# Kernel optimization log

Hardware: AMD Instinct MI355X
Metric: run time of the kernel (lower is better)

The kernel has to match this reference:

```python
import jax, jax.numpy as jnp
import numpy as np
import math

B = 2; T = 512; ND = 256; NDAYS = 24; STRIDE = 4; KLEN = 14
DM = ND * KLEN          # 3584, d_model after unfolding
NLAYERS = 2; DSTATE = 16; DCONV = 4; EXPAND = 2
DI = EXPAND * DM        # 7168 d_inner
DTR = math.ceil(DM / 16)  # 224 dt_rank
NCLS = 41
LOUT = (T - KLEN) // STRIDE + 1  # 125


def setup_inputs():
    key = jax.random.key(0)
    ks = jax.random.split(key, 12)
    f32 = jnp.float32
    neuralInput = jax.random.normal(ks[0], (B, T, ND), f32)
    dayIdx = jax.random.randint(ks[1], (B,), 0, NDAYS)
    # day-specific linear init: identity weight, zero bias (as in BaseDecoder)
    day_w = jnp.tile(jnp.eye(ND, dtype=f32)[None], (NDAYS, 1, 1))
    day_b = jnp.zeros((NDAYS, 1, ND), f32)
    norm_w = jnp.ones((NLAYERS, DM), f32)
    norm_b = jnp.zeros((NLAYERS, DM), f32)
    in_proj_w = 0.02 * jax.random.normal(ks[2], (NLAYERS, 2 * DI, DM), f32)
    conv_w = 0.2 * jax.random.normal(ks[3], (NLAYERS, DI, DCONV), f32)  # depthwise
    conv_b = jnp.zeros((NLAYERS, DI), f32)
    x_proj_w = 0.02 * jax.random.normal(ks[4], (NLAYERS, DTR + 2 * DSTATE, DI), f32)
    s = DTR ** -0.5
    dt_proj_w = jax.random.uniform(ks[5], (NLAYERS, DI, DTR), f32, -s, s)
    # dt bias init: inverse-softplus of dt ~ LogUniform[1e-3, 1e-1]
    dt = jnp.exp(jax.random.uniform(ks[6], (NLAYERS, DI), f32) * (math.log(0.1) - math.log(0.001)) + math.log(0.001))
    dt = jnp.clip(dt, 1e-4, None)
    dt_proj_b = dt + jnp.log(-jnp.expm1(-dt))
    A_log = jnp.broadcast_to(jnp.log(jnp.arange(1, DSTATE + 1, dtype=f32)), (NLAYERS, DI, DSTATE)).copy()
    D_param = jnp.ones((NLAYERS, DI), f32)
    out_proj_w = 0.02 * jax.random.normal(ks[7], (NLAYERS, DM, DI), f32)
    normf_w = jnp.ones((DM,), f32)
    normf_b = jnp.zeros((DM,), f32)
    fc_w = 0.02 * jax.random.normal(ks[8], (NCLS, DM), f32)
    fc_b = jnp.zeros((NCLS,), f32)
    return dict(neuralInput=neuralInput, day_w=day_w, day_b=day_b, norm_w=norm_w, norm_b=norm_b,
                in_proj_w=in_proj_w, conv_w=conv_w, conv_b=conv_b, x_proj_w=x_proj_w,
                dt_proj_w=dt_proj_w, dt_proj_b=dt_proj_b, A_log=A_log, D_param=D_param,
                out_proj_w=out_proj_w, normf_w=normf_w, normf_b=normf_b, fc_w=fc_w, fc_b=fc_b,
                dayIdx=dayIdx)


def _layernorm(x, w, b):
    mu = x.mean(-1, keepdims=True)
    v = jnp.var(x, -1, keepdims=True)
    return (x - mu) * jax.lax.rsqrt(v + 1e-5) * w + b


def _mamba(h, ipw, cw, cb, xpw, dtw, dtb, Alog, Dp, opw):
    # h: (B, L, DM) -> (B, L, DM); unidirectional Mamba, use_fast_path=False math
    Bb, L, _ = h.shape
    xz = h @ ipw.T                              # (B, L, 2*DI)
    x, z = xz[..., :DI], xz[..., DI:]
    # depthwise causal conv1d, kernel DCONV, left pad DCONV-1, truncated to L
    xp = jnp.pad(x, ((0, 0), (DCONV - 1, 0), (0, 0)))
    xc = cb + sum(xp[:, j:j + L, :] * cw[:, j] for j in range(DCONV))
    x = jax.nn.silu(xc)
    x_dbl = x @ xpw.T                           # (B, L, DTR + 2*N)
    dt = x_dbl[..., :DTR]
    Bc = x_dbl[..., DTR:DTR + DSTATE]
    Cc = x_dbl[..., DTR + DSTATE:]
    delta = jax.nn.softplus(dt @ dtw.T + dtb)   # (B, L, DI), delta_softplus=True
    A = -jnp.exp(Alog)                          # (DI, N)
    dA = jnp.exp(delta[..., None] * A)          # (B, L, DI, N)
    dBu = (delta * x)[..., None] * Bc[:, :, None, :]  # (B, L, DI, N)

    def step(hst, inp):
        a, bu, c = inp
        hst = a * hst + bu                      # (B, DI, N)
        return hst, jnp.einsum('bdn,bn->bd', hst, c)

    h0 = jnp.zeros((Bb, DI, DSTATE), h.dtype)
    _, ys = jax.lax.scan(step, h0, (dA.transpose(1, 0, 2, 3), dBu.transpose(1, 0, 2, 3), Cc.transpose(1, 0, 2)))
    y = ys.transpose(1, 0, 2) + x * Dp          # skip term D*u
    y = y * jax.nn.silu(z)                      # gated output
    return y @ opw.T


def reference(neuralInput, day_w, day_b, norm_w, norm_b, in_proj_w, conv_w, conv_b, x_proj_w,
              dt_proj_w, dt_proj_b, A_log, D_param, out_proj_w, normf_w, normf_b, fc_w, fc_b, dayIdx):
    # --- BaseDecoder.forward_preprocessing (gaussianSmoothWidth = 0) ---
    t = jnp.einsum('btd,bdk->btk', neuralInput, day_w[dayIdx]) + day_b[dayIdx]
    t = t / (1.0 + jnp.abs(t))                  # Softsign
    idx = jnp.arange(LOUT)[:, None] * STRIDE + jnp.arange(KLEN)[None, :]
    win = t[:, idx, :]                          # (B, LOUT, KLEN, ND)
    # torch Unfold feature ordering: channel-major then kernel position -> d*KLEN + j
    h = win.transpose(0, 1, 3, 2).reshape(t.shape[0], LOUT, DM)
    # --- stacked Mamba blocks (pre-norm residual) ---
    residual = None
    for i in range(NLAYERS):
        residual = h if residual is None else h + residual
        hn = _layernorm(residual, norm_w[i], norm_b[i])
        h = _mamba(hn, in_proj_w[i], conv_w[i], conv_b[i], x_proj_w[i], dt_proj_w[i],
                   dt_proj_b[i], A_log[i], D_param[i], out_proj_w[i])
    residual = h + residual
    hn = _layernorm(residual, normf_w, normf_b)
    return hn @ fc_w.T + fc_b                   # (B, LOUT, NCLS)
```

## Files before the change

### kernel.cpp

```cpp
#include <hip/hip_runtime.h>
#include <hip/hip_bf16.h>
#include <math.h>

#define BATCH   2
#define TSEQ    512
#define NDIM    256
#define STRIDE_ 4
#define KLEN    14
#define DM      3584
#define DI      7168
#define DTR     224
#define DSTATE  16
#define NCLS    41
#define LOUT    125
#define LPAD    128
#define MROWS   256

typedef __attribute__((ext_vector_type(8))) short bf8_t;
typedef __attribute__((ext_vector_type(4))) float f4_t;

__device__ inline unsigned bfpair(float a, float b) {
    unsigned ua = __builtin_bit_cast(unsigned, a);
    unsigned ub = __builtin_bit_cast(unsigned, b);
    ua = (ua + 0x7fffu + ((ua >> 16) & 1u)) >> 16;
    ub = (ub + 0x7fffu + ((ub >> 16) & 1u)) >> 16;
    return ua | (ub << 16);
}
__device__ inline uint4 pack8(float4 a, float4 b) {
    return make_uint4(bfpair(a.x, a.y), bfpair(a.z, a.w),
                      bfpair(b.x, b.y), bfpair(b.z, b.w));
}

__global__ void day_proj(const float* __restrict__ nI, const float* __restrict__ dw,
                         const float* __restrict__ db, const int* __restrict__ dayIdx,
                         float* __restrict__ t_full) {
    int bi = blockIdx.x;
    int b = bi >> 9;
    int di = dayIdx[b];
    int tid = threadIdx.x;
    __shared__ float a_sh[256];
    a_sh[tid] = nI[(size_t)bi * 256 + tid];
    __syncthreads();
    const float* w = dw + (size_t)di * 65536;
    float acc = db[(size_t)di * 256 + tid];
    #pragma unroll 8
    for (int d = 0; d < 256; ++d) acc = fmaf(a_sh[d], w[d * 256 + tid], acc);
    t_full[(size_t)bi * 256 + tid] = acc / (1.f + fabsf(acc));
}

__global__ void window_k(const float* __restrict__ t_full, float* __restrict__ res) {
    int bl = blockIdx.x;
    int b = bl >> 7, l = bl & 127;
    size_t m = (size_t)b * LPAD + l;
    if (l >= LOUT) {
        for (int c = threadIdx.x; c < DM; c += 256) res[m * DM + c] = 0.f;
        return;
    }
    for (int c = threadIdx.x; c < DM; c += 256) {
        int d = c / KLEN, j = c - d * KLEN;
        res[m * DM + c] = t_full[((size_t)b * TSEQ + l * STRIDE_ + j) * 256 + d];
    }
}

__global__ void ln_pack(const float* __restrict__ res, const float* __restrict__ w,
                        const float* __restrict__ b, short* __restrict__ hnp) {
    int m = blockIdx.x, tid = threadIdx.x;
    const float* row = res + (size_t)m * DM;
    float s = 0.f, ss = 0.f;
    for (int c = tid; c < DM; c += 256) { float v = row[c]; s += v; ss += v * v; }
    #pragma unroll
    for (int o = 32; o; o >>= 1) { s += __shfl_xor(s, o); ss += __shfl_xor(ss, o); }
    __shared__ float sm[8];
    int wid = tid >> 6;
    if ((tid & 63) == 0) { sm[wid] = s; sm[4 + wid] = ss; }
    __syncthreads();
    s = sm[0] + sm[1] + sm[2] + sm[3];
    ss = sm[4] + sm[5] + sm[6] + sm[7];
    float mu = s * (1.f / DM);
    float var = ss * (1.f / DM) - mu * mu;
    float rs = rsqrtf(var + 1e-5f);
    for (int G = tid; G < DM / 8; G += 256) {
        float4 f0 = *(const float4*)(row + G * 8);
        float4 f1 = *(const float4*)(row + G * 8 + 4);
        float4 w0 = *(const float4*)(w + G * 8);
        float4 w1 = *(const float4*)(w + G * 8 + 4);
        float4 b0 = *(const float4*)(b + G * 8);
        float4 b1 = *(const float4*)(b + G * 8 + 4);
        f0.x = (f0.x - mu) * rs * w0.x + b0.x; f0.y = (f0.y - mu) * rs * w0.y + b0.y;
        f0.z = (f0.z - mu) * rs * w0.z + b0.z; f0.w = (f0.w - mu) * rs * w0.w + b0.w;
        f1.x = (f1.x - mu) * rs * w1.x + b1.x; f1.y = (f1.y - mu) * rs * w1.y + b1.y;
        f1.z = (f1.z - mu) * rs * w1.z + b1.z; f1.w = (f1.w - mu) * rs * w1.w + b1.w;
        *(uint4*)&hnp[((size_t)G * 256 + m) * 8] = pack8(f0, f1);
    }
}

__global__ void pack_rows(const float* __restrict__ src, int lda, int nG,
                          short* __restrict__ dst) {
    int m = blockIdx.x;
    const float* row = src + (size_t)m * lda;
    for (int G = threadIdx.x; G < nG; G += 256) {
        float4 f0 = *(const float4*)(row + G * 8);
        float4 f1 = *(const float4*)(row + G * 8 + 4);
        *(uint4*)&dst[((size_t)G * 256 + m) * 8] = pack8(f0, f1);
    }
}

__global__ void zero_k(float* __restrict__ p) {
    size_t i = (size_t)(blockIdx.x * 256 + threadIdx.x) * 4;
    *(float4*)(p + i) = make_float4(0.f, 0.f, 0.f, 0.f);
}

template <int EPI>
__global__ __launch_bounds__(256)
void gemm_mfma(const short* __restrict__ Ap, const float* __restrict__ W, int ldw,
               float* __restrict__ C, int ldc, int kSteps,
               const float* __restrict__ bias) {
    __shared__ __align__(16) short a_sh[2][4][2056];
    __shared__ __align__(16) short w_sh[2][4][520];
    const int tid = threadIdx.x;
    const int wz = tid >> 6, lane = tid & 63;
    const int g = lane >> 4, i16 = lane & 15;
    const int n0 = blockIdx.x * 64;
    const int sBeg = blockIdx.z * kSteps, sEnd = sBeg + kSteps;
    const int wr = tid >> 3;
    const int wq = tid & 7;

    f4_t acc[4][4];
    #pragma unroll
    for (int r = 0; r < 4; ++r)
        #pragma unroll
        for (int c = 0; c < 4; ++c) acc[r][c] = (f4_t){0.f, 0.f, 0.f, 0.f};

    const short* arow = Ap + (size_t)tid * 8;
    const float* wbase  = W + (size_t)(n0 + wr) * ldw + wq * 4;
    const float* wbase2 = wbase + (size_t)32 * ldw;

    float4 wv0 = *(const float4*)(wbase  + (size_t)sBeg * 32);
    float4 wv1 = *(const float4*)(wbase2 + (size_t)sBeg * 32);
    #pragma unroll
    for (int it = 0; it < 4; ++it)
        __builtin_amdgcn_global_load_lds(
            (const __attribute__((address_space(1))) unsigned int*)(arow + (size_t)(sBeg * 4 + it) * 2048),
            (__attribute__((address_space(3))) unsigned int*)&a_sh[0][it][tid * 8], 16, 0, 0);
    {
        uint2 p0 = {bfpair(wv0.x, wv0.y), bfpair(wv0.z, wv0.w)};
        *(uint2*)&w_sh[0][wq >> 1][wr * 8 + (wq & 1) * 4] = p0;
        uint2 p1 = {bfpair(wv1.x, wv1.y), bfpair(wv1.z, wv1.w)};
        *(uint2*)&w_sh[0][wq >> 1][(wr + 32) * 8 + (wq & 1) * 4] = p1;
    }
    int s1 = (sBeg + 1 < sEnd) ? sBeg + 1 : sEnd - 1;
    wv0 = *(const float4*)(wbase  + (size_t)s1 * 32);
    wv1 = *(const float4*)(wbase2 + (size_t)s1 * 32);

    for (int s = sBeg; s < sEnd; ++s) {
        const int cur = (s - sBeg) & 1, nxt = cur ^ 1;
        __syncthreads();
        if (s + 1 < sEnd) {
            #pragma unroll
            for (int it = 0; it < 4; ++it)
                __builtin_amdgcn_global_load_lds(
                    (const __attribute__((address_space(1))) unsigned int*)(arow + (size_t)((s + 1) * 4 + it) * 2048),
                    (__attribute__((address_space(3))) unsigned int*)&a_sh[nxt][it][tid * 8], 16, 0, 0);
            uint2 p0 = {bfpair(wv0.x, wv0.y), bfpair(wv0.z, wv0.w)};
            *(uint2*)&w_sh[nxt][wq >> 1][wr * 8 + (wq & 1) * 4] = p0;
            uint2 p1 = {bfpair(wv1.x, wv1.y), bfpair(wv1.z, wv1.w)};
            *(uint2*)&w_sh[nxt][wq >> 1][(wr + 32) * 8 + (wq & 1) * 4] = p1;
            int s2 = (s + 2 < sEnd) ? s + 2 : sEnd - 1;
            wv0 = *(const float4*)(wbase  + (size_t)s2 * 32);
            wv1 = *(const float4*)(wbase2 + (size_t)s2 * 32);
        }
        bf8_t af[4], wf[4];
        #pragma unroll
        for (int r = 0; r < 4; ++r)
            af[r] = *(const bf8_t*)&a_sh[cur][g][(wz * 64 + r * 16 + i16) * 8];
        #pragma unroll
        for (int c = 0; c < 4; ++c)
            wf[c] = *(const bf8_t*)&w_sh[cur][g][(c * 16 + i16) * 8];
        #pragma unroll
        for (int r = 0; r < 4; ++r)
            #pragma unroll
            for (int c = 0; c < 4; ++c)
                acc[r][c] = __builtin_amdgcn_mfma_f32_16x16x32_bf16(af[r], wf[c], acc[r][c], 0, 0, 0);
    }

    float bv[4];
    if (EPI == 1) {
        #pragma unroll
        for (int c = 0; c < 4; ++c) bv[c] = bias[n0 + c * 16 + i16];
    }
    #pragma unroll
    for (int r = 0; r < 4; ++r) {
        #pragma unroll
        for (int c = 0; c < 4; ++c) {
            int n = n0 + c * 16 + i16;
            #pragma unroll
            for (int v = 0; v < 4; ++v) {
                int m = wz * 64 + r * 16 + g * 4 + v;
                float val = acc[r][c][v];
                if (EPI == 0) {
                    C[(size_t)m * ldc + n] = val;
                } else if (EPI == 1) {
                    val += bv[c];
                    C[(size_t)m * ldc + n] = (val > 20.f) ? val : log1pf(expf(val));
                } else {
                    atomicAdd(&C[(size_t)m * ldc + n], val);
                }
            }
        }
    }
}

__global__ void conv_silu_pack(const float* __restrict__ xz, const float* __restrict__ cw,
                               const float* __restrict__ cb, float* __restrict__ xq,
                               short* __restrict__ xqp) {
    int bl = blockIdx.x;
    int b = bl / 125, l = bl % 125;
    size_t m = (size_t)b * LPAD + l;
    for (int c0 = threadIdx.x * 8; c0 < DI; c0 += 2048) {
        float v[8];
        float4 cb0 = *(const float4*)(cb + c0);
        float4 cb1 = *(const float4*)(cb + c0 + 4);
        v[0] = cb0.x; v[1] = cb0.y; v[2] = cb0.z; v[3] = cb0.w;
        v[4] = cb1.x; v[5] = cb1.y; v[6] = cb1.z; v[7] = cb1.w;
        #pragma unroll
        for (int j = 0; j < 4; ++j) {
            int lj = l - 3 + j;
            if (lj < 0) continue;
            const float* xr = xz + ((size_t)b * LPAD + lj) * (2 * DI) + c0;
            float4 x0 = *(const float4*)xr;
            float4 x1 = *(const float4*)(xr + 4);
            float xa[8] = {x0.x, x0.y, x0.z, x0.w, x1.x, x1.y, x1.z, x1.w};
            #pragma unroll
            for (int k = 0; k < 8; ++k)
                v[k] = fmaf(xa[k], cw[(c0 + k) * 4 + j], v[k]);
        }
        float4 o0, o1;
        #pragma unroll
        for (int k = 0; k < 8; ++k) {
            float sv = v[k] / (1.f + expf(-v[k]));
            if (k < 4) (&o0.x)[k] = sv; else (&o1.x)[k - 4] = sv;
        }
        *(float4*)(xq + m * DI + c0) = o0;
        *(float4*)(xq + m * DI + c0 + 4) = o1;
        *(uint4*)&xqp[(((size_t)c0 / 8) * 256 + m) * 8] = pack8(o0, o1);
    }
}

union F16u { float4 v4[4]; float f[16]; };

__global__ void scan_kernel(const float* __restrict__ delta, const float* __restrict__ xq,
                            const float* __restrict__ xdbl, const float* __restrict__ xz,
                            const float* __restrict__ Alog, const float* __restrict__ Dp,
                            float* __restrict__ y) {
    int c = blockIdx.x * 256 + threadIdx.x;
    int b = blockIdx.y;
    float As[DSTATE], st[DSTATE];
    #pragma unroll
    for (int s = 0; s < DSTATE; ++s) {
        As[s] = -expf(Alog[(size_t)c * DSTATE + s]);
        st[s] = 0.f;
    }
    float dp = Dp[c];
    size_t mb = (size_t)b * LPAD;
    float d_c = delta[mb * DI + c];
    float x_c = xq[mb * DI + c];
    float z_c = xz[mb * (2 * DI) + DI + c];
    F16u B_c, C_c;
    {
        const float4* p = (const float4*)(xdbl + mb * 256 + DTR);
        B_c.v4[0] = p[0]; B_c.v4[1] = p[1]; B_c.v4[2] = p[2]; B_c.v4[3] = p[3];
        C_c.v4[0] = p[4]; C_c.v4[1] = p[5]; C_c.v4[2] = p[6]; C_c.v4[3] = p[7];
    }
    for (int l = 0; l < LOUT; ++l) {
        float d_n = d_c, x_n = x_c, z_n = z_c;
        F16u B_n = B_c, C_n = C_c;
        if (l + 1 < LOUT) {
            size_t m = mb + l + 1;
            d_n = delta[m * DI + c];
            x_n = xq[m * DI + c];
            z_n = xz[m * (2 * DI) + DI + c];
            const float4* p = (const float4*)(xdbl + m * 256 + DTR);
            B_n.v4[0] = p[0]; B_n.v4[1] = p[1]; B_n.v4[2] = p[2]; B_n.v4[3] = p[3];
            C_n.v4[0] = p[4]; C_n.v4[1] = p[5]; C_n.v4[2] = p[6]; C_n.v4[3] = p[7];
        }
        float du = d_c * x_c;
        float yv = 0.f;
        #pragma unroll
        for (int s = 0; s < DSTATE; ++s) {
            st[s] = fmaf(expf(d_c * As[s]), st[s], du * B_c.f[s]);
            yv = fmaf(st[s], C_c.f[s], yv);
        }
        y[(mb + l) * DI + c] = (yv + x_c * dp) * (z_c / (1.f + expf(-z_c)));
        d_c = d_n; x_c = x_n; z_c = z_n; B_c = B_n; C_c = C_n;
    }
}

__global__ void ln_fc(const float* __restrict__ res, const float* __restrict__ wf,
                      const float* __restrict__ bf, const float* __restrict__ fcw,
                      const float* __restrict__ fcb, float* __restrict__ out) {
    __shared__ __align__(16) float hs[DM];
    __shared__ float sm[8];
    int bl = blockIdx.x;
    int b = bl / 125, l = bl % 125;
    size_t m = (size_t)b * LPAD + l;
    int tid = threadIdx.x;
    const float* row = res + m * DM;
    float s = 0.f, ss = 0.f;
    for (int c = tid; c < DM; c += 256) { float v = row[c]; s += v; ss += v * v; }
    #pragma unroll
    for (int o = 32; o; o >>= 1) { s += __shfl_xor(s, o); ss += __shfl_xor(ss, o); }
    int wid = tid >> 6;
    if ((tid & 63) == 0) { sm[wid] = s; sm[4 + wid] = ss; }
    __syncthreads();
    s = sm[0] + sm[1] + sm[2] + sm[3];
    ss = sm[4] + sm[5] + sm[6] + sm[7];
    float mu = s * (1.f / DM);
    float var = ss * (1.f / DM) - mu * mu;
    float rs = rsqrtf(var + 1e-5f);
    for (int c = tid; c < DM; c += 256) hs[c] = (row[c] - mu) * rs * wf[c] + bf[c];
    __syncthreads();
    int lane = tid & 63;
    for (int n = wid; n < NCLS; n += 4) {
        const float* wrow = fcw + (size_t)n * DM;
        float a0 = 0.f, a1 = 0.f, a2 = 0.f, a3 = 0.f;
        for (int k = lane; k < DM; k += 256) {
            a0 = fmaf(hs[k],       wrow[k],       a0);
            a1 = fmaf(hs[k + 64],  wrow[k + 64],  a1);
            a2 = fmaf(hs[k + 128], wrow[k + 128], a2);
            a3 = fmaf(hs[k + 192], wrow[k + 192], a3);
        }
        float acc = (a0 + a1) + (a2 + a3);
        #pragma unroll
        for (int o = 32; o; o >>= 1) acc += __shfl_xor(acc, o);
        if (lane == 0) out[((size_t)b * LOUT + l) * NCLS + n] = acc + fcb[n];
    }
}

extern "C" void kernel_launch(void* const* d_in, const int* in_sizes, int n_in,
                              void* d_out, int out_size, void* d_ws, size_t ws_size,
                              hipStream_t stream) {
    (void)in_sizes; (void)n_in; (void)out_size; (void)ws_size;
    const float* nI   = (const float*)d_in[0];
    const float* dw   = (const float*)d_in[1];
    const float* db   = (const float*)d_in[2];
    const float* nw   = (const float*)d_in[3];
    const float* nb   = (const float*)d_in[4];
    const float* ipw  = (const float*)d_in[5];
    const float* cw   = (const float*)d_in[6];
    const float* cb   = (const float*)d_in[7];
    const float* xpw  = (const float*)d_in[8];
    const float* dtw  = (const float*)d_in[9];
    const float* dtb  = (const float*)d_in[10];
    const float* Alog = (const float*)d_in[11];
    const float* Dp   = (const float*)d_in[12];
    const float* opw  = (const float*)d_in[13];
    const float* nfw  = (const float*)d_in[14];
    const float* nfb  = (const float*)d_in[15];
    const float* fcw  = (const float*)d_in[16];
    const float* fcb  = (const float*)d_in[17];
    const int*   dayI = (const int*)d_in[18];
    float* out = (float*)d_out;

    float* wsf = (float*)d_ws;
    float* t_full = wsf; wsf += 262144;
    float* res    = wsf; wsf += (size_t)MROWS * DM;
    float* xz     = wsf; wsf += (size_t)MROWS * 2 * DI;
    float* xq     = wsf; wsf += (size_t)MROWS * DI;
    float* xdbl   = wsf; wsf += (size_t)MROWS * 256;
    float* delta  = wsf; wsf += (size_t)MROWS * DI;
    float* yb     = wsf; wsf += (size_t)MROWS * DI;
    short* wss = (short*)wsf;
    short* hnp   = wss; wss += (size_t)MROWS * DM;
    short* xqp   = wss; wss += (size_t)MROWS * DI;
    short* xdblp = wss; wss += (size_t)MROWS * DTR;
    short* ybp   = wss; wss += (size_t)MROWS * DI;

    day_proj<<<dim3(BATCH * TSEQ), 256, 0, stream>>>(nI, dw, db, dayI, t_full);
    window_k<<<dim3(MROWS), 256, 0, stream>>>(t_full, res);

    for (int i = 0; i < 2; ++i) {
        ln_pack<<<dim3(MROWS), 256, 0, stream>>>(res, nw + (size_t)i * DM, nb + (size_t)i * DM, hnp);
        gemm_mfma<0><<<dim3(224, 1, 1), 256, 0, stream>>>(
            hnp, ipw + (size_t)i * 2 * DI * DM, DM, xz, 2 * DI, 112, nullptr);
        conv_silu_pack<<<dim3(BATCH * LOUT), 256, 0, stream>>>(
            xz, cw + (size_t)i * DI * 4, cb + (size_t)i * DI, xq, xqp);
        zero_k<<<dim3(64), 256, 0, stream>>>(xdbl);
        gemm_mfma<2><<<dim3(4, 1, 28), 256, 0, stream>>>(
            xqp, xpw + (size_t)i * 256 * DI, DI, xdbl, 256, 8, nullptr);
        pack_rows<<<dim3(MROWS), 256, 0, stream>>>(xdbl, 256, DTR / 8, xdblp);
        gemm_mfma<1><<<dim3(112, 1, 1), 256, 0, stream>>>(
            xdblp, dtw + (size_t)i * DI * DTR, DTR, delta, DI, 7, dtb + (size_t)i * DI);
        scan_kernel<<<dim3(DI / 256, BATCH), 256, 0, stream>>>(
            delta, xq, xdbl, xz, Alog + (size_t)i * DI * DSTATE, Dp + (size_t)i * DI, yb);
        pack_rows<<<dim3(MROWS), 256, 0, stream>>>(yb, DI, DI / 8, ybp);
        gemm_mfma<2><<<dim3(56, 1, 8), 256, 0, stream>>>(
            ybp, opw + (size_t)i * DM * DI, DI, res, DM, 28, nullptr);
    }

    ln_fc<<<dim3(BATCH * LOUT), 256, 0, stream>>>(res, nfw, nfb, fcw, fcb, out);
}
```

Before: 1.353 ms.

## Halve GEMM N-tile to 32 and split scan states across four threads

The MFMA GEMM gets an N-tile template parameter. All GEMMs now use 32-column tiles with twice as many blocks, and the out_proj split-K is reduced from 8 to 4. The selective scan now gives each channel's 16 states to 4 threads, which combine their partial outputs with shuffles, so it launches four times as many threads. Both changes aim to fill the GPU's compute units better on these small-M problems, at the cost of more weight-tile redundancy, lower MFMA work per block, and extra shuffle and load overhead in the scan.

```diff
diff --git a/kernel.cpp b/kernel.cpp
--- a/kernel.cpp
+++ b/kernel.cpp
@@ -110,33 +110,35 @@
     *(float4*)(p + i) = make_float4(0.f, 0.f, 0.f, 0.f);
 }
 
-template <int EPI>
+template <int EPI, int NT>
 __global__ __launch_bounds__(256)
 void gemm_mfma(const short* __restrict__ Ap, const float* __restrict__ W, int ldw,
                float* __restrict__ C, int ldc, int kSteps,
                const float* __restrict__ bias) {
+    constexpr int NC = NT / 16;
     __shared__ __align__(16) short a_sh[2][4][2056];
-    __shared__ __align__(16) short w_sh[2][4][520];
+    __shared__ __align__(16) short w_sh[2][4][NT * 8 + 8];
     const int tid = threadIdx.x;
     const int wz = tid >> 6, lane = tid & 63;
     const int g = lane >> 4, i16 = lane & 15;
-    const int n0 = blockIdx.x * 64;
+    const int n0 = blockIdx.x * NT;
     const int sBeg = blockIdx.z * kSteps, sEnd = sBeg + kSteps;
     const int wr = tid >> 3;
     const int wq = tid & 7;
 
-    f4_t acc[4][4];
+    f4_t acc[4][NC];
     #pragma unroll
     for (int r = 0; r < 4; ++r)
         #pragma unroll
-        for (int c = 0; c < 4; ++c) acc[r][c] = (f4_t){0.f, 0.f, 0.f, 0.f};
+        for (int c = 0; c < NC; ++c) acc[r][c] = (f4_t){0.f, 0.f, 0.f, 0.f};
 
     const short* arow = Ap + (size_t)tid * 8;
     const float* wbase  = W + (size_t)(n0 + wr) * ldw + wq * 4;
     const float* wbase2 = wbase + (size_t)32 * ldw;
 
-    float4 wv0 = *(const float4*)(wbase  + (size_t)sBeg * 32);
-    float4 wv1 = *(const float4*)(wbase2 + (size_t)sBeg * 32);
+    float4 wv0 = *(const float4*)(wbase + (size_t)sBeg * 32);
+    float4 wv1;
+    if constexpr (NT == 64) wv1 = *(const float4*)(wbase2 + (size_t)sBeg * 32);
     #pragma unroll
     for (int it = 0; it < 4; ++it)
         __builtin_amdgcn_global_load_lds(
@@ -145,12 +147,14 @@
     {
         uint2 p0 = {bfpair(wv0.x, wv0.y), bfpair(wv0.z, wv0.w)};
         *(uint2*)&w_sh[0][wq >> 1][wr * 8 + (wq & 1) * 4] = p0;
-        uint2 p1 = {bfpair(wv1.x, wv1.y), bfpair(wv1.z, wv1.w)};
-        *(uint2*)&w_sh[0][wq >> 1][(wr + 32) * 8 + (wq & 1) * 4] = p1;
+        if constexpr (NT == 64) {
+            uint2 p1 = {bfpair(wv1.x, wv1.y), bfpair(wv1.z, wv1.w)};
+            *(uint2*)&w_sh[0][wq >> 1][(wr + 32) * 8 + (wq & 1) * 4] = p1;
+        }
     }
     int s1 = (sBeg + 1 < sEnd) ? sBeg + 1 : sEnd - 1;
-    wv0 = *(const float4*)(wbase  + (size_t)s1 * 32);
-    wv1 = *(const float4*)(wbase2 + (size_t)s1 * 32);
+    wv0 = *(const float4*)(wbase + (size_t)s1 * 32);
+    if constexpr (NT == 64) wv1 = *(const float4*)(wbase2 + (size_t)s1 * 32);
 
     for (int s = sBeg; s < sEnd; ++s) {
         const int cur = (s - sBeg) & 1, nxt = cur ^ 1;
@@ -163,35 +167,37 @@
                     (__attribute__((address_space(3))) unsigned int*)&a_sh[nxt][it][tid * 8], 16, 0, 0);
             uint2 p0 = {bfpair(wv0.x, wv0.y), bfpair(wv0.z, wv0.w)};
             *(uint2*)&w_sh[nxt][wq >> 1][wr * 8 + (wq & 1) * 4] = p0;
-            uint2 p1 = {bfpair(wv1.x, wv1.y), bfpair(wv1.z, wv1.w)};
-            *(uint2*)&w_sh[nxt][wq >> 1][(wr + 32) * 8 + (wq & 1) * 4] = p1;
+            if constexpr (NT == 64) {
+                uint2 p1 = {bfpair(wv1.x, wv1.y), bfpair(wv1.z, wv1.w)};
+                *(uint2*)&w_sh[nxt][wq >> 1][(wr + 32) * 8 + (wq & 1) * 4] = p1;
+            }
             int s2 = (s + 2 < sEnd) ? s + 2 : sEnd - 1;
-            wv0 = *(const float4*)(wbase  + (size_t)s2 * 32);
-            wv1 = *(const float4*)(wbase2 + (size_t)s2 * 32);
-        }
-        bf8_t af[4], wf[4];
+            wv0 = *(const float4*)(wbase + (size_t)s2 * 32);
+            if constexpr (NT == 64) wv1 = *(const float4*)(wbase2 + (size_t)s2 * 32);
+        }
+        bf8_t af[4], wf[NC];
         #pragma unroll
         for (int r = 0; r < 4; ++r)
             af[r] = *(const bf8_t*)&a_sh[cur][g][(wz * 64 + r * 16 + i16) * 8];
         #pragma unroll
-        for (int c = 0; c < 4; ++c)
+        for (int c = 0; c < NC; ++c)
             wf[c] = *(const bf8_t*)&w_sh[cur][g][(c * 16 + i16) * 8];
         #pragma unroll
         for (int r = 0; r < 4; ++r)
             #pragma unroll
-            for (int c = 0; c < 4; ++c)
+            for (int c = 0; c < NC; ++c)
                 acc[r][c] = __builtin_amdgcn_mfma_f32_16x16x32_bf16(af[r], wf[c], acc[r][c], 0, 0, 0);
     }
 
-    float bv[4];
+    float bv[NC];
     if (EPI == 1) {
         #pragma unroll
-        for (int c = 0; c < 4; ++c) bv[c] = bias[n0 + c * 16 + i16];
+        for (int c = 0; c < NC; ++c) bv[c] = bias[n0 + c * 16 + i16];
     }
     #pragma unroll
     for (int r = 0; r < 4; ++r) {
         #pragma unroll
-        for (int c = 0; c < 4; ++c) {
+        for (int c = 0; c < NC; ++c) {
             int n = n0 + c * 16 + i16;
             #pragma unroll
             for (int v = 0; v < 4; ++v) {
@@ -246,51 +252,49 @@
     }
 }
 
-union F16u { float4 v4[4]; float f[16]; };
-
 __global__ void scan_kernel(const float* __restrict__ delta, const float* __restrict__ xq,
                             const float* __restrict__ xdbl, const float* __restrict__ xz,
                             const float* __restrict__ Alog, const float* __restrict__ Dp,
                             float* __restrict__ y) {
-    int c = blockIdx.x * 256 + threadIdx.x;
+    int tid = threadIdx.x;
+    int sg = tid & 3;
+    int c = blockIdx.x * 64 + (tid >> 2);
     int b = blockIdx.y;
-    float As[DSTATE], st[DSTATE];
-    #pragma unroll
-    for (int s = 0; s < DSTATE; ++s) {
-        As[s] = -expf(Alog[(size_t)c * DSTATE + s]);
-        st[s] = 0.f;
+    float As[4], st[4];
+    #pragma unroll
+    for (int k = 0; k < 4; ++k) {
+        As[k] = -expf(Alog[(size_t)c * DSTATE + sg * 4 + k]);
+        st[k] = 0.f;
     }
     float dp = Dp[c];
     size_t mb = (size_t)b * LPAD;
     float d_c = delta[mb * DI + c];
     float x_c = xq[mb * DI + c];
     float z_c = xz[mb * (2 * DI) + DI + c];
-    F16u B_c, C_c;
-    {
-        const float4* p = (const float4*)(xdbl + mb * 256 + DTR);
-        B_c.v4[0] = p[0]; B_c.v4[1] = p[1]; B_c.v4[2] = p[2]; B_c.v4[3] = p[3];
-        C_c.v4[0] = p[4]; C_c.v4[1] = p[5]; C_c.v4[2] = p[6]; C_c.v4[3] = p[7];
-    }
+    float4 B_c = *(const float4*)(xdbl + mb * 256 + DTR + sg * 4);
+    float4 C_c = *(const float4*)(xdbl + mb * 256 + DTR + DSTATE + sg * 4);
     for (int l = 0; l < LOUT; ++l) {
         float d_n = d_c, x_n = x_c, z_n = z_c;
-        F16u B_n = B_c, C_n = C_c;
+        float4 B_n = B_c, C_n = C_c;
         if (l + 1 < LOUT) {
             size_t m = mb + l + 1;
             d_n = delta[m * DI + c];
             x_n = xq[m * DI + c];
             z_n = xz[m * (2 * DI) + DI + c];
-            const float4* p = (const float4*)(xdbl + m * 256 + DTR);
-            B_n.v4[0] = p[0]; B_n.v4[1] = p[1]; B_n.v4[2] = p[2]; B_n.v4[3] = p[3];
-            C_n.v4[0] = p[4]; C_n.v4[1] = p[5]; C_n.v4[2] = p[6]; C_n.v4[3] = p[7];
+            B_n = *(const float4*)(xdbl + m * 256 + DTR + sg * 4);
+            C_n = *(const float4*)(xdbl + m * 256 + DTR + DSTATE + sg * 4);
         }
         float du = d_c * x_c;
         float yv = 0.f;
         #pragma unroll
-        for (int s = 0; s < DSTATE; ++s) {
-            st[s] = fmaf(expf(d_c * As[s]), st[s], du * B_c.f[s]);
-            yv = fmaf(st[s], C_c.f[s], yv);
-        }
-        y[(mb + l) * DI + c] = (yv + x_c * dp) * (z_c / (1.f + expf(-z_c)));
+        for (int k = 0; k < 4; ++k) {
+            st[k] = fmaf(expf(d_c * As[k]), st[k], du * (&B_c.x)[k]);
+            yv = fmaf(st[k], (&C_c.x)[k], yv);
+        }
+        yv += __shfl_xor(yv, 1);
+        yv += __shfl_xor(yv, 2);
+        if (sg == 0)
+            y[(mb + l) * DI + c] = (yv + x_c * dp) * (z_c / (1.f + expf(-z_c)));
         d_c = d_n; x_c = x_n; z_c = z_n; B_c = B_n; C_c = C_n;
     }
 }
@@ -380,21 +384,21 @@
 
     for (int i = 0; i < 2; ++i) {
         ln_pack<<<dim3(MROWS), 256, 0, stream>>>(res, nw + (size_t)i * DM, nb + (size_t)i * DM, hnp);
-        gemm_mfma<0><<<dim3(224, 1, 1), 256, 0, stream>>>(
+        gemm_mfma<0, 32><<<dim3(448, 1, 1), 256, 0, stream>>>(
             hnp, ipw + (size_t)i * 2 * DI * DM, DM, xz, 2 * DI, 112, nullptr);
         conv_silu_pack<<<dim3(BATCH * LOUT), 256, 0, stream>>>(
             xz, cw + (size_t)i * DI * 4, cb + (size_t)i * DI, xq, xqp);
         zero_k<<<dim3(64), 256, 0, stream>>>(xdbl);
-        gemm_mfma<2><<<dim3(4, 1, 28), 256, 0, stream>>>(
+        gemm_mfma<2, 32><<<dim3(8, 1, 28), 256, 0, stream>>>(
             xqp, xpw + (size_t)i * 256 * DI, DI, xdbl, 256, 8, nullptr);
         pack_rows<<<dim3(MROWS), 256, 0, stream>>>(xdbl, 256, DTR / 8, xdblp);
-        gemm_mfma<1><<<dim3(112, 1, 1), 256, 0, stream>>>(
+        gemm_mfma<1, 32><<<dim3(224, 1, 1), 256, 0, stream>>>(
             xdblp, dtw + (size_t)i * DI * DTR, DTR, delta, DI, 7, dtb + (size_t)i * DI);
-        scan_kernel<<<dim3(DI / 256, BATCH), 256, 0, stream>>>(
+        scan_kernel<<<dim3(DI / 64, BATCH), 256, 0, stream>>>(
             delta, xq, xdbl, xz, Alog + (size_t)i * DI * DSTATE, Dp + (size_t)i * DI, yb);
         pack_rows<<<dim3(MROWS), 256, 0, stream>>>(yb, DI, DI / 8, ybp);
-        gemm_mfma<2><<<dim3(56, 1, 8), 256, 0, stream>>>(
-            ybp, opw + (size_t)i * DM * DI, DI, res, DM, 28, nullptr);
+        gemm_mfma<2, 32><<<dim3(112, 1, 4), 256, 0, stream>>>(
+            ybp, opw + (size_t)i * DM * DI, DI, res, DM, 56, nullptr);
     }
 
     ln_fc<<<dim3(BATCH * LOUT), 256, 0, stream>>>(res, nfw, nfb, fcw, fcb, out);
```

After: 1.381 ms. +2.1%, slower.
